# Kernel optimization log

Hardware: AMD Instinct MI355X
Metric: run time of the kernel (lower is better)

## Reference

```python
import jax, jax.numpy as jnp
import numpy as np

N_QUBITS = 8
N_LAYERS = 4
DIM = 2 ** N_QUBITS
C64 = jnp.complex64
ROTS = ['RX', 'RY', 'RZ']

# PauliZ sign table: wire 0 is the most-significant bit (PennyLane convention).
_bits = (np.arange(DIM)[:, None] >> (N_QUBITS - 1 - np.arange(N_QUBITS))[None, :]) & 1
Z_SIGNS = jnp.asarray(1.0 - 2.0 * _bits, dtype=jnp.float32)  # (DIM, n_qubits)


def _apply_1q(state, gate, q):
    """Apply a 2x2 gate (or batched (B,2,2) gate) on qubit q. state: (B, DIM) complex64."""
    L = 2 ** q
    R = DIM // (2 * L)
    s = state.reshape(-1, L, 2, R)
    if gate.ndim == 3:
        s = jnp.einsum('bij,bljr->blir', gate, s)
    else:
        s = jnp.einsum('ij,bljr->blir', gate, s)
    return s.reshape(-1, DIM)


def _apply_cnot(state, q):
    """CNOT with control q, target q+1 (adjacent wires): permute basis states."""
    L = 2 ** q
    R = DIM // (4 * L)
    perm = jnp.array([0, 1, 3, 2])
    s = state.reshape(-1, L, 4, R)[:, :, perm, :]
    return s.reshape(-1, DIM)


def _rot(name, t):
    """Scalar-angle single-qubit rotation gate, 2x2 complex64."""
    h = 0.5 * t
    c = jnp.cos(h).astype(C64)
    s = jnp.sin(h).astype(C64)
    if name == 'RX':
        return jnp.stack([jnp.stack([c, -1j * s]), jnp.stack([-1j * s, c])])
    if name == 'RY':
        return jnp.stack([jnp.stack([c, -s]), jnp.stack([s, c])])
    e = jnp.exp(-1j * h).astype(C64)  # RZ = diag(e^{-it/2}, e^{+it/2})
    z = jnp.zeros((), C64)
    return jnp.stack([jnp.stack([e, z]), jnp.stack([z, jnp.conj(e)])])


def _circuit(enc, theta):
    """enc: (B, n_qubits) real angles; theta: (n_layers, n_qubits, 3). Returns <Z_q>: (B, n_qubits)."""
    B = enc.shape[0]
    state = jnp.zeros((B, DIM), C64).at[:, 0].set(1.0)
    # Angle encoding: RY(enc[:, q]) on each wire (batched gate).
    for q in range(N_QUBITS):
        h = 0.5 * enc[:, q]
        c, s = jnp.cos(h), jnp.sin(h)
        g = jnp.stack([jnp.stack([c, -s], -1), jnp.stack([s, c], -1)], -2).astype(C64)
        state = _apply_1q(state, g, q)
    # PCE ansatz: per layer RX/RY/RZ on every qubit, then brickwall CNOT entanglement.
    for l in range(N_LAYERS):
        for q in range(N_QUBITS):
            for r, name in enumerate(ROTS):
                state = _apply_1q(state, _rot(name, theta[l, q, r]), q)
        for i in range(l % 2, N_QUBITS - 1, 2):
            state = _apply_cnot(state, i)
    probs = state.real ** 2 + state.imag ** 2          # (B, DIM)
    return probs @ Z_SIGNS                              # (B, n_qubits)


def setup_inputs() -> dict:
    key = jax.random.key(0)
    k1, k2, k3, k4 = jax.random.split(key, 4)
    B, D_IN, D_OUT = 8192, 512, 512
    x = jax.random.normal(k1, (B, D_IN), dtype=jnp.float32)
    W_in = jax.random.normal(k2, (N_QUBITS, D_IN), dtype=jnp.float32) * (1.0 / np.sqrt(D_IN))
    W_out = jax.random.normal(k3, (D_OUT, N_QUBITS), dtype=jnp.float32) * (1.0 / np.sqrt(N_QUBITS))
    theta = jax.random.normal(k4, (N_LAYERS, N_QUBITS, 3), dtype=jnp.float32) * 0.1
    return {"x": x, "W_in": W_in, "W_out": W_out, "theta": theta}


def reference(x, W_in, W_out, theta):
    enc = jnp.tanh(x @ W_in.T) * jnp.pi     # (B, n_qubits), encoded angles
    z = _circuit(enc, theta)                # (B, n_qubits), PauliZ expvals
    return z @ W_out.T                      # (B, output_dim)
```

## Files before the change

### kernel.cpp

```cpp
#include <hip/hip_runtime.h>
#include <hip/hip_bf16.h>
#include <math.h>


#define BTS 288
#define PSIS 288

typedef __attribute__((ext_vector_type(8))) short bf16x8;
typedef __attribute__((ext_vector_type(4))) float f32x4;

__device__ __forceinline__ float2 shfl_xor_f2(float2 v, int m) {
  float2 r;
  r.x = __shfl_xor(v.x, m, 64);
  r.y = __shfl_xor(v.y, m, 64);
  return r;
}
__device__ __forceinline__ float2 cfma(float2 u, float2 v, float2 acc) {
  acc.x = fmaf(u.x, v.x, fmaf(-u.y, v.y, acc.x));
  acc.y = fmaf(u.x, v.y, fmaf(u.y, v.x, acc.y));
  return acc;
}

__device__ __forceinline__ void apply_gate(float2 (&a)[4], int q, float2 u00,
                                           float2 u01, float2 u10, float2 u11,
                                           int lane) {
  const float2 z0 = make_float2(0.f, 0.f);
  if (q == 7) {
    float2 n0 = cfma(u00, a[0], cfma(u01, a[1], z0));
    float2 n1 = cfma(u10, a[0], cfma(u11, a[1], z0));
    float2 n2 = cfma(u00, a[2], cfma(u01, a[3], z0));
    float2 n3 = cfma(u10, a[2], cfma(u11, a[3], z0));
    a[0] = n0; a[1] = n1; a[2] = n2; a[3] = n3;
  } else if (q == 6) {
    float2 n0 = cfma(u00, a[0], cfma(u01, a[2], z0));
    float2 n2 = cfma(u10, a[0], cfma(u11, a[2], z0));
    float2 n1 = cfma(u00, a[1], cfma(u01, a[3], z0));
    float2 n3 = cfma(u10, a[1], cfma(u11, a[3], z0));
    a[0] = n0; a[1] = n1; a[2] = n2; a[3] = n3;
  } else {
    int m = 1 << (5 - q);
    bool b = (lane >> (5 - q)) & 1;
    float2 ca = b ? u11 : u00;
    float2 cp = b ? u10 : u01;
    #pragma unroll
    for (int k = 0; k < 4; ++k) {
      float2 p = shfl_xor_f2(a[k], m);
      a[k] = cfma(ca, a[k], cfma(cp, p, z0));
    }
  }
}

__device__ __forceinline__ void apply_cnot(float2 (&a)[4], int q, int lane) {
  if (q <= 4) {
    int m = 1 << (4 - q);
    bool ctrl = (lane >> (5 - q)) & 1;
    #pragma unroll
    for (int k = 0; k < 4; ++k) {
      float2 p = shfl_xor_f2(a[k], m);
      a[k].x = ctrl ? p.x : a[k].x;
      a[k].y = ctrl ? p.y : a[k].y;
    }
  } else if (q == 5) {
    bool ct = lane & 1;
    float2 n0 = ct ? a[2] : a[0];
    float2 n1 = ct ? a[3] : a[1];
    float2 n2 = ct ? a[0] : a[2];
    float2 n3 = ct ? a[1] : a[3];
    a[0] = n0; a[1] = n1; a[2] = n2; a[3] = n3;
  } else {
    float2 t = a[2]; a[2] = a[3]; a[3] = t;
  }
}

__global__ __launch_bounds__(256) void k01_kernel(
    const float* __restrict__ x, const float* __restrict__ W_in,
    const float* __restrict__ theta, __hip_bfloat16* __restrict__ Bt,
    __hip_bfloat16* __restrict__ psi, int B) {
  __shared__ float mats[32 * 8];
  const int tid = threadIdx.x;
  const int lane = tid & 63;

  if (blockIdx.x < 64) {
    if (tid < 32) {
      int l = tid >> 3, q = tid & 7;
      const float* th = theta + (l * 8 + q) * 3;
      float h1 = 0.5f * th[0], h2 = 0.5f * th[1], h3 = 0.5f * th[2];
      float c1 = cosf(h1), s1 = sinf(h1);
      float c2 = cosf(h2), s2 = sinf(h2);
      float c3 = cosf(h3), s3 = sinf(h3);
      float m00r = c2 * c1, m00i = s2 * s1;
      float m01r = -s2 * c1, m01i = -c2 * s1;
      float m10r = s2 * c1, m10i = -c2 * s1;
      float m11r = c1 * c2, m11i = -s1 * s2;
      float* o = &mats[tid * 8];
      o[0] = c3 * m00r + s3 * m00i;  o[1] = c3 * m00i - s3 * m00r;
      o[2] = c3 * m01r + s3 * m01i;  o[3] = c3 * m01i - s3 * m01r;
      o[4] = c3 * m10r - s3 * m10i;  o[5] = c3 * m10i + s3 * m10r;
      o[6] = c3 * m11r - s3 * m11i;  o[7] = c3 * m11i + s3 * m11r;
    }
    __syncthreads();

    const int j = blockIdx.x * 4 + (tid >> 6);
    float2 a[4];
    #pragma unroll
    for (int k = 0; k < 4; ++k)
      a[k] = make_float2((lane * 4 + k == j) ? 1.f : 0.f, 0.f);

    #pragma unroll
    for (int l = 0; l < 4; ++l) {
      #pragma unroll
      for (int q = 0; q < 8; ++q) {
        const float* m = &mats[(l * 8 + q) * 8];
        float2 u00 = make_float2(m[0], m[1]);
        float2 u01 = make_float2(m[2], m[3]);
        float2 u10 = make_float2(m[4], m[5]);
        float2 u11 = make_float2(m[6], m[7]);
        apply_gate(a, q, u00, u01, u10, u11, lane);
      }
      #pragma unroll
      for (int i = (l & 1); i < 7; i += 2) apply_cnot(a, i, lane);
    }
    #pragma unroll
    for (int k = 0; k < 4; ++k) {
      int n0 = (lane * 4 + k) * 2;
      Bt[n0 * BTS + j]       = __float2bfloat16(a[k].x);
      Bt[(n0 + 1) * BTS + j] = __float2bfloat16(a[k].y);
    }
    return;
  }

  const int b = (int)(blockIdx.x - 64) * 4 + (tid >> 6);
  if (b >= B) return;

  float xv[8];
  #pragma unroll
  for (int j = 0; j < 8; ++j) xv[j] = x[b * 512 + j * 64 + lane];

  float acc[8];
  #pragma unroll
  for (int q = 0; q < 8; ++q) {
    float s = 0.f;
    #pragma unroll
    for (int j = 0; j < 8; ++j)
      s = fmaf(xv[j], W_in[q * 512 + j * 64 + lane], s);
    acc[q] = s;
  }
  #pragma unroll
  for (int m = 1; m < 64; m <<= 1) {
    #pragma unroll
    for (int q = 0; q < 8; ++q) acc[q] += __shfl_xor(acc[q], m, 64);
  }

  float cq[8], sq[8];
  #pragma unroll
  for (int q = 0; q < 8; ++q) {
    float e  = __expf(2.f * acc[q]);
    float th = 1.f - __fdividef(2.f, e + 1.f);
    float h  = 1.57079632679489662f * th;
    cq[q] = __cosf(h);
    sq[q] = __sinf(h);
  }

  float base = 1.f;
  #pragma unroll
  for (int q = 0; q < 6; ++q)
    base *= ((lane >> (5 - q)) & 1) ? sq[q] : cq[q];

  float a0 = base * cq[6] * cq[7];
  float a1 = base * cq[6] * sq[7];
  float a2 = base * sq[6] * cq[7];
  float a3 = base * sq[6] * sq[7];

  __hip_bfloat16 h4[4] = {__float2bfloat16(a0), __float2bfloat16(a1),
                          __float2bfloat16(a2), __float2bfloat16(a3)};
  uint2 pk = *reinterpret_cast<uint2*>(h4);
  *reinterpret_cast<uint2*>(psi + (size_t)b * PSIS + lane * 4) = pk;
}

__global__ __launch_bounds__(256, 1) void k2_kernel(
    const __hip_bfloat16* __restrict__ psi, const __hip_bfloat16* __restrict__ Bt,
    const float* __restrict__ W_out, float* __restrict__ out) {
  __shared__ float z_lds[4][32][8];
  __shared__ float z_final[32][8];
  const int tid = threadIdx.x;
  const int lane = tid & 63;
  const int w = tid >> 6;
  const int rowbase = blockIdx.x * 32;
  const int cl = lane & 15;
  const int kg = lane >> 4;

  const short* psis = (const short*)psi;
  const short* Bts  = (const short*)Bt;

  bf16x8 Af[2][8];
  #pragma unroll
  for (int rt = 0; rt < 2; ++rt)
    #pragma unroll
    for (int kb = 0; kb < 8; ++kb)
      Af[rt][kb] = *(const bf16x8*)(psis +
          (size_t)(rowbase + rt * 16 + cl) * PSIS + kb * 32 + kg * 8);

  const int wcol = w * 128;
  f32x4 acc[2][8];
  #pragma unroll
  for (int rt = 0; rt < 2; ++rt)
    #pragma unroll
    for (int ct = 0; ct < 8; ++ct) acc[rt][ct] = (f32x4){0.f, 0.f, 0.f, 0.f};

  #pragma unroll
  for (int ct = 0; ct < 8; ++ct) {
    const short* bp = Bts + (size_t)(wcol + ct * 16 + cl) * BTS + kg * 8;
    bf16x8 Bf[8];
    #pragma unroll
    for (int kb = 0; kb < 8; ++kb) Bf[kb] = *(const bf16x8*)(bp + kb * 32);
    #pragma unroll
    for (int kb = 0; kb < 8; ++kb) {
      acc[0][ct] = __builtin_amdgcn_mfma_f32_16x16x32_bf16(Af[0][kb], Bf[kb],
                                                           acc[0][ct], 0, 0, 0);
      acc[1][ct] = __builtin_amdgcn_mfma_f32_16x16x32_bf16(Af[1][kb], Bf[kb],
                                                           acc[1][ct], 0, 0, 0);
    }
  }

  float zacc[2][4][4];
  #pragma unroll
  for (int rt = 0; rt < 2; ++rt)
    #pragma unroll
    for (int u = 0; u < 4; ++u)
      #pragma unroll
      for (int jr = 0; jr < 4; ++jr) zacc[rt][u][jr] = 0.f;

  #pragma unroll
  for (int ct = 0; ct < 8; ++ct) {
    int n = wcol + ct * 16 + cl;
    int i = n >> 1;
    int ib = (lane & 1) ? (i & 15) : (i >> 4);
    float s[4];
    #pragma unroll
    for (int u = 0; u < 4; ++u)
      s[u] = ((ib >> (3 - u)) & 1) ? -1.f : 1.f;
    #pragma unroll
    for (int rt = 0; rt < 2; ++rt) {
      #pragma unroll
      for (int jr = 0; jr < 4; ++jr) {
        float v = acc[rt][ct][jr];
        v = v * v;
        float P = v + __shfl_xor(v, 1, 64);
        #pragma unroll
        for (int u = 0; u < 4; ++u)
          zacc[rt][u][jr] = fmaf(s[u], P, zacc[rt][u][jr]);
      }
    }
  }

  #pragma unroll
  for (int m = 2; m <= 8; m <<= 1)
    #pragma unroll
    for (int rt = 0; rt < 2; ++rt)
      #pragma unroll
      for (int u = 0; u < 4; ++u)
        #pragma unroll
        for (int jr = 0; jr < 4; ++jr)
          zacc[rt][u][jr] += __shfl_xor(zacc[rt][u][jr], m, 64);

  if (cl <= 1) {
    #pragma unroll
    for (int rt = 0; rt < 2; ++rt)
      #pragma unroll
      for (int u = 0; u < 4; ++u)
        #pragma unroll
        for (int jr = 0; jr < 4; ++jr)
          z_lds[w][rt * 16 + kg * 4 + jr][(lane & 1) * 4 + u] = zacc[rt][u][jr];
  }
  __syncthreads();

  {
    int r = tid >> 3, q = tid & 7;
    z_final[r][q] = z_lds[0][r][q] + z_lds[1][r][q] + z_lds[2][r][q] +
                    z_lds[3][r][q];
  }
  __syncthreads();

  const int o0 = tid, o1 = 256 + tid;
  float4 wa0 = *(const float4*)(W_out + o0 * 8);
  float4 wb0 = *(const float4*)(W_out + o0 * 8 + 4);
  float4 wa1 = *(const float4*)(W_out + o1 * 8);
  float4 wb1 = *(const float4*)(W_out + o1 * 8 + 4);
  #pragma unroll 4
  for (int r = 0; r < 32; ++r) {
    float4 z0 = *(const float4*)&z_final[r][0];
    float4 z1 = *(const float4*)&z_final[r][4];
    float d0 = wa0.x * z0.x + wa0.y * z0.y + wa0.z * z0.z + wa0.w * z0.w +
               wb0.x * z1.x + wb0.y * z1.y + wb0.z * z1.z + wb0.w * z1.w;
    float d1 = wa1.x * z0.x + wa1.y * z0.y + wa1.z * z0.z + wa1.w * z0.w +
               wb1.x * z1.x + wb1.y * z1.y + wb1.z * z1.z + wb1.w * z1.w;
    out[(size_t)(rowbase + r) * 512 + o0] = d0;
    out[(size_t)(rowbase + r) * 512 + o1] = d1;
  }
}

extern "C" void kernel_launch(void* const* d_in, const int* in_sizes, int n_in,
                              void* d_out, int out_size, void* d_ws, size_t ws_size,
                              hipStream_t stream) {
  const float* x     = (const float*)d_in[0];
  const float* W_in  = (const float*)d_in[1];
  const float* W_out = (const float*)d_in[2];
  const float* theta = (const float*)d_in[3];
  float* out = (float*)d_out;

  const int B = in_sizes[0] / 512;
  const size_t btBytes = (size_t)512 * BTS * sizeof(__hip_bfloat16);

  __hip_bfloat16* Bt  = (__hip_bfloat16*)d_ws;
  __hip_bfloat16* psi = (__hip_bfloat16*)((char*)d_ws + btBytes);

  hipLaunchKernelGGL(k01_kernel, dim3(64 + B / 4), dim3(256), 0, stream,
                     x, W_in, theta, Bt, psi, B);
  hipLaunchKernelGGL(k2_kernel, dim3(B / 32), dim3(256), 0, stream,
                     psi, Bt, W_out, out);
}
```

Before: 34.04 us.

## Fold PauliZ signs and W_out into a bf16 hi/lo matrix applied via MFMA

Builds a combined matrix M[o,i] = sum_q sign(i,q) * W_out[o,q] in extra blocks of the first kernel, stored as a bf16 hi/lo split. The second kernel writes the probabilities to LDS as bf16 and runs a second MFMA GEMM (P @ M) straight to the output. This replaces the shuffle reductions, the cross-wave z reduction and the scalar W_out dot products. In exchange it does extra MFMA work, reads more global memory for M, and loses precision because the probabilities are quantised to bf16.

```diff
diff --git a/kernel.cpp b/kernel.cpp
--- a/kernel.cpp
+++ b/kernel.cpp
@@ -4,10 +4,23 @@
 
 
 #define BTS 288
+#define MTS 288
 #define PSIS 288
+#define PLS 296
 
 typedef __attribute__((ext_vector_type(8))) short bf16x8;
 typedef __attribute__((ext_vector_type(4))) float f32x4;
+
+static __device__ __forceinline__ unsigned short f2bf(float f) {
+  __hip_bfloat16 h = __float2bfloat16(f);
+  return *reinterpret_cast<unsigned short*>(&h);
+}
+static __device__ __forceinline__ float bf2f(unsigned short u) {
+  unsigned int v = ((unsigned int)u) << 16;
+  float r;
+  __builtin_memcpy(&r, &v, 4);
+  return r;
+}
 
 __device__ __forceinline__ float2 shfl_xor_f2(float2 v, int m) {
   float2 r;
@@ -74,8 +87,10 @@
 
 __global__ __launch_bounds__(256) void k01_kernel(
     const float* __restrict__ x, const float* __restrict__ W_in,
-    const float* __restrict__ theta, __hip_bfloat16* __restrict__ Bt,
-    __hip_bfloat16* __restrict__ psi, int B) {
+    const float* __restrict__ W_out, const float* __restrict__ theta,
+    __hip_bfloat16* __restrict__ Bt, unsigned short* __restrict__ Mthi,
+    unsigned short* __restrict__ Mtlo, __hip_bfloat16* __restrict__ psi,
+    int B) {
   __shared__ float mats[32 * 8];
   const int tid = threadIdx.x;
   const int lane = tid & 63;
@@ -111,11 +126,8 @@
       #pragma unroll
       for (int q = 0; q < 8; ++q) {
         const float* m = &mats[(l * 8 + q) * 8];
-        float2 u00 = make_float2(m[0], m[1]);
-        float2 u01 = make_float2(m[2], m[3]);
-        float2 u10 = make_float2(m[4], m[5]);
-        float2 u11 = make_float2(m[6], m[7]);
-        apply_gate(a, q, u00, u01, u10, u11, lane);
+        apply_gate(a, q, make_float2(m[0], m[1]), make_float2(m[2], m[3]),
+                   make_float2(m[4], m[5]), make_float2(m[6], m[7]), lane);
       }
       #pragma unroll
       for (int i = (l & 1); i < 7; i += 2) apply_cnot(a, i, lane);
@@ -129,7 +141,29 @@
     return;
   }
 
-  const int b = (int)(blockIdx.x - 64) * 4 + (tid >> 6);
+  if (blockIdx.x < 72) {
+    const int bb = (int)blockIdx.x - 64;
+    const int o = bb * 64 + (tid >> 2);
+    const int seg = tid & 3;
+    float wq[8];
+    #pragma unroll
+    for (int q = 0; q < 8; ++q) wq[q] = W_out[o * 8 + q];
+    #pragma unroll 8
+    for (int ii = 0; ii < 64; ++ii) {
+      int i = seg * 64 + ii;
+      float s = 0.f;
+      #pragma unroll
+      for (int q = 0; q < 8; ++q)
+        s += ((i >> (7 - q)) & 1) ? -wq[q] : wq[q];
+      unsigned short h = f2bf(s);
+      unsigned short l = f2bf(s - bf2f(h));
+      Mthi[o * MTS + i] = h;
+      Mtlo[o * MTS + i] = l;
+    }
+    return;
+  }
+
+  const int b = (int)(blockIdx.x - 72) * 4 + (tid >> 6);
   if (b >= B) return;
 
   float xv[8];
@@ -166,28 +200,27 @@
   for (int q = 0; q < 6; ++q)
     base *= ((lane >> (5 - q)) & 1) ? sq[q] : cq[q];
 
-  float a0 = base * cq[6] * cq[7];
-  float a1 = base * cq[6] * sq[7];
-  float a2 = base * sq[6] * cq[7];
-  float a3 = base * sq[6] * sq[7];
-
-  __hip_bfloat16 h4[4] = {__float2bfloat16(a0), __float2bfloat16(a1),
-                          __float2bfloat16(a2), __float2bfloat16(a3)};
+  __hip_bfloat16 h4[4];
+  h4[0] = __float2bfloat16(base * cq[6] * cq[7]);
+  h4[1] = __float2bfloat16(base * cq[6] * sq[7]);
+  h4[2] = __float2bfloat16(base * sq[6] * cq[7]);
+  h4[3] = __float2bfloat16(base * sq[6] * sq[7]);
   uint2 pk = *reinterpret_cast<uint2*>(h4);
   *reinterpret_cast<uint2*>(psi + (size_t)b * PSIS + lane * 4) = pk;
 }
 
 __global__ __launch_bounds__(256, 1) void k2_kernel(
     const __hip_bfloat16* __restrict__ psi, const __hip_bfloat16* __restrict__ Bt,
-    const float* __restrict__ W_out, float* __restrict__ out) {
-  __shared__ float z_lds[4][32][8];
-  __shared__ float z_final[32][8];
+    const unsigned short* __restrict__ Mthi,
+    const unsigned short* __restrict__ Mtlo, float* __restrict__ out) {
+  __shared__ unsigned short P_lds[32 * PLS];
   const int tid = threadIdx.x;
   const int lane = tid & 63;
   const int w = tid >> 6;
   const int rowbase = blockIdx.x * 32;
   const int cl = lane & 15;
   const int kg = lane >> 4;
+  const int wcol = w * 128;
 
   const short* psis = (const short*)psi;
   const short* Bts  = (const short*)Bt;
@@ -200,7 +233,6 @@
       Af[rt][kb] = *(const bf16x8*)(psis +
           (size_t)(rowbase + rt * 16 + cl) * PSIS + kb * 32 + kg * 8);
 
-  const int wcol = w * 128;
   f32x4 acc[2][8];
   #pragma unroll
   for (int rt = 0; rt < 2; ++rt)
@@ -222,23 +254,10 @@
     }
   }
 
-  float zacc[2][4][4];
-  #pragma unroll
-  for (int rt = 0; rt < 2; ++rt)
-    #pragma unroll
-    for (int u = 0; u < 4; ++u)
-      #pragma unroll
-      for (int jr = 0; jr < 4; ++jr) zacc[rt][u][jr] = 0.f;
-
+  const bool wr = (cl & 1) == 0;
+  const int ibase = (wcol >> 1) + (cl >> 1);
   #pragma unroll
   for (int ct = 0; ct < 8; ++ct) {
-    int n = wcol + ct * 16 + cl;
-    int i = n >> 1;
-    int ib = (lane & 1) ? (i & 15) : (i >> 4);
-    float s[4];
-    #pragma unroll
-    for (int u = 0; u < 4; ++u)
-      s[u] = ((ib >> (3 - u)) & 1) ? -1.f : 1.f;
     #pragma unroll
     for (int rt = 0; rt < 2; ++rt) {
       #pragma unroll
@@ -246,56 +265,59 @@
         float v = acc[rt][ct][jr];
         v = v * v;
         float P = v + __shfl_xor(v, 1, 64);
-        #pragma unroll
-        for (int u = 0; u < 4; ++u)
-          zacc[rt][u][jr] = fmaf(s[u], P, zacc[rt][u][jr]);
+        if (wr) {
+          int row = rt * 16 + kg * 4 + jr;
+          P_lds[row * PLS + ibase + ct * 8] = f2bf(P);
+        }
       }
     }
   }
-
-  #pragma unroll
-  for (int m = 2; m <= 8; m <<= 1)
-    #pragma unroll
-    for (int rt = 0; rt < 2; ++rt)
-      #pragma unroll
-      for (int u = 0; u < 4; ++u)
-        #pragma unroll
-        for (int jr = 0; jr < 4; ++jr)
-          zacc[rt][u][jr] += __shfl_xor(zacc[rt][u][jr], m, 64);
-
-  if (cl <= 1) {
-    #pragma unroll
-    for (int rt = 0; rt < 2; ++rt)
-      #pragma unroll
-      for (int u = 0; u < 4; ++u)
-        #pragma unroll
-        for (int jr = 0; jr < 4; ++jr)
-          z_lds[w][rt * 16 + kg * 4 + jr][(lane & 1) * 4 + u] = zacc[rt][u][jr];
-  }
   __syncthreads();
 
-  {
-    int r = tid >> 3, q = tid & 7;
-    z_final[r][q] = z_lds[0][r][q] + z_lds[1][r][q] + z_lds[2][r][q] +
-                    z_lds[3][r][q];
-  }
-  __syncthreads();
-
-  const int o0 = tid, o1 = 256 + tid;
-  float4 wa0 = *(const float4*)(W_out + o0 * 8);
-  float4 wb0 = *(const float4*)(W_out + o0 * 8 + 4);
-  float4 wa1 = *(const float4*)(W_out + o1 * 8);
-  float4 wb1 = *(const float4*)(W_out + o1 * 8 + 4);
-  #pragma unroll 4
-  for (int r = 0; r < 32; ++r) {
-    float4 z0 = *(const float4*)&z_final[r][0];
-    float4 z1 = *(const float4*)&z_final[r][4];
-    float d0 = wa0.x * z0.x + wa0.y * z0.y + wa0.z * z0.z + wa0.w * z0.w +
-               wb0.x * z1.x + wb0.y * z1.y + wb0.z * z1.z + wb0.w * z1.w;
-    float d1 = wa1.x * z0.x + wa1.y * z0.y + wa1.z * z0.z + wa1.w * z0.w +
-               wb1.x * z1.x + wb1.y * z1.y + wb1.z * z1.z + wb1.w * z1.w;
-    out[(size_t)(rowbase + r) * 512 + o0] = d0;
-    out[(size_t)(rowbase + r) * 512 + o1] = d1;
+  bf16x8 Pf[2][8];
+  #pragma unroll
+  for (int rt = 0; rt < 2; ++rt)
+    #pragma unroll
+    for (int kb = 0; kb < 8; ++kb)
+      Pf[rt][kb] = *(const bf16x8*)((const short*)P_lds +
+          (rt * 16 + cl) * PLS + kb * 32 + kg * 8);
+
+  f32x4 acc3[2][8];
+  #pragma unroll
+  for (int rt = 0; rt < 2; ++rt)
+    #pragma unroll
+    for (int ct = 0; ct < 8; ++ct) acc3[rt][ct] = (f32x4){0.f, 0.f, 0.f, 0.f};
+
+  const short* Mhs = (const short*)Mthi;
+  const short* Mls = (const short*)Mtlo;
+  #pragma unroll
+  for (int ct = 0; ct < 8; ++ct) {
+    const size_t mo = (size_t)(wcol + ct * 16 + cl) * MTS + kg * 8;
+    #pragma unroll
+    for (int kb = 0; kb < 8; ++kb) {
+      bf16x8 mh = *(const bf16x8*)(Mhs + mo + kb * 32);
+      bf16x8 ml = *(const bf16x8*)(Mls + mo + kb * 32);
+      acc3[0][ct] = __builtin_amdgcn_mfma_f32_16x16x32_bf16(Pf[0][kb], mh,
+                                                            acc3[0][ct], 0, 0, 0);
+      acc3[0][ct] = __builtin_amdgcn_mfma_f32_16x16x32_bf16(Pf[0][kb], ml,
+                                                            acc3[0][ct], 0, 0, 0);
+      acc3[1][ct] = __builtin_amdgcn_mfma_f32_16x16x32_bf16(Pf[1][kb], mh,
+                                                            acc3[1][ct], 0, 0, 0);
+      acc3[1][ct] = __builtin_amdgcn_mfma_f32_16x16x32_bf16(Pf[1][kb], ml,
+                                                            acc3[1][ct], 0, 0, 0);
+    }
+  }
+
+  #pragma unroll
+  for (int ct = 0; ct < 8; ++ct) {
+    #pragma unroll
+    for (int rt = 0; rt < 2; ++rt) {
+      #pragma unroll
+      for (int jr = 0; jr < 4; ++jr) {
+        int row = rowbase + rt * 16 + kg * 4 + jr;
+        out[(size_t)row * 512 + wcol + ct * 16 + cl] = acc3[rt][ct][jr];
+      }
+    }
   }
 }
 
@@ -309,13 +331,15 @@
   float* out = (float*)d_out;
 
   const int B = in_sizes[0] / 512;
-  const size_t btBytes = (size_t)512 * BTS * sizeof(__hip_bfloat16);
-
-  __hip_bfloat16* Bt  = (__hip_bfloat16*)d_ws;
-  __hip_bfloat16* psi = (__hip_bfloat16*)((char*)d_ws + btBytes);
-
-  hipLaunchKernelGGL(k01_kernel, dim3(64 + B / 4), dim3(256), 0, stream,
-                     x, W_in, theta, Bt, psi, B);
+  const size_t matBytes = (size_t)512 * 288 * sizeof(short);
+
+  __hip_bfloat16* Bt   = (__hip_bfloat16*)d_ws;
+  unsigned short* Mthi = (unsigned short*)((char*)d_ws + matBytes);
+  unsigned short* Mtlo = (unsigned short*)((char*)d_ws + 2 * matBytes);
+  __hip_bfloat16* psi  = (__hip_bfloat16*)((char*)d_ws + 3 * matBytes);
+
+  hipLaunchKernelGGL(k01_kernel, dim3(72 + B / 4), dim3(256), 0, stream,
+                     x, W_in, W_out, theta, Bt, Mthi, Mtlo, psi, B);
   hipLaunchKernelGGL(k2_kernel, dim3(B / 32), dim3(256), 0, stream,
-                     psi, Bt, W_out, out);
-}
+                     psi, Bt, Mthi, Mtlo, out);
+}
```

Measured after the change: 50.17 us. +47.4%, slower.
